# Performance work log

Measured on AMD Instinct MI355X. Metric: run time of the kernel, lower is better.

Reference implementation:

```python
import jax, jax.numpy as jnp
import numpy as np

N_TOKENS = 4096
EMBED = 2048
D_ATTN = 2048


def setup_inputs() -> dict:
    key = jax.random.key(0)
    k1, k2, k3, k4 = jax.random.split(key, 4)
    # torch.rand -> uniform [0,1); keeps scores positive so the multiplicative
    # -inf mask acts as a clean causal mask (faithful to original behavior).
    token_embeddings = jax.random.uniform(k1, (N_TOKENS, EMBED), dtype=jnp.float32)
    W_Q = jax.random.uniform(k2, (EMBED, D_ATTN), dtype=jnp.float32)
    W_K = jax.random.uniform(k3, (EMBED, D_ATTN), dtype=jnp.float32)
    W_V = jax.random.uniform(k4, (EMBED, D_ATTN), dtype=jnp.float32)
    return {"token_embeddings": token_embeddings, "W_Q": W_Q, "W_K": W_K, "W_V": W_V}


def reference(token_embeddings, W_Q, W_K, W_V):
    n = token_embeddings.shape[0]
    d = W_Q.shape[1]
    # mask: 1 on/below diagonal, -inf strictly above (multiplicative, as in source)
    neg_inf = jnp.float32(-jnp.inf)
    mask = jnp.tril(jnp.ones((n, n), dtype=jnp.float32)) + jnp.triu(
        jnp.full((n, n), neg_inf, dtype=jnp.float32), k=1
    )
    Q = token_embeddings @ W_Q          # (n, d)
    K = token_embeddings @ W_K          # (n, d)
    V = token_embeddings @ W_V          # (n, d)
    scores = (Q @ K.T) * mask           # (n, n); upper tri -> -inf (scores > 0)
    scores = scores / jnp.sqrt(jnp.float32(d))
    attn = jax.nn.softmax(scores, axis=-1)
    return attn @ V                     # (n, d)
```

## Files before the change

### kernel.cpp

```cpp
#include <hip/hip_runtime.h>
#include <hip/hip_bf16.h>
#include <cstdint>
#include <cstddef>
#include <cmath>

#define N_TOK 4096
#define EMB   2048
#define DATT  2048

typedef __attribute__((ext_vector_type(8))) short short8;
typedef __attribute__((ext_vector_type(4))) short shortx4;
typedef __attribute__((ext_vector_type(4))) float f32x4;

#define MFMA(a, b, c) __builtin_amdgcn_mfma_f32_16x16x32_bf16(a, b, c, 0, 0, 0)

__device__ __forceinline__ short f2bs(float f) {
  __hip_bfloat16 h = __float2bfloat16(f);
  return __builtin_bit_cast(short, h);
}
__device__ __forceinline__ float bs2f(short s) {
  return __uint_as_float(((unsigned)(unsigned short)s) << 16);
}
__device__ __forceinline__ float ldin(const void* p, size_t i, int isbf) {
  if (isbf) {
    unsigned short u = ((const unsigned short*)p)[i];
    return __uint_as_float(((unsigned int)u) << 16);
  }
  return ((const float*)p)[i];
}

__device__ __forceinline__ size_t swz(int r, int c, int kdim) {
  return ((size_t)((r >> 7) * (kdim >> 3) + (c >> 3)) << 10) +
         (size_t)((r & 127) << 3) + (c & 7);
}

__device__ __forceinline__ void gl16(const short* g, short* l) {
  __builtin_amdgcn_global_load_lds(
      (const __attribute__((address_space(1))) unsigned int*)(const void*)g,
      (__attribute__((address_space(3))) unsigned int*)(void*)l, 16, 0, 0);
}

template <bool THREE>
__device__ __forceinline__ void gemm_core(const short* Ah, const short* Al,
                                          const short* Bh, const short* Bl,
                                          int chunks, int apan, int bpan,
                                          int kmax, short* lds,
                                          f32x4 acc[4][4]) {
  const int NSL = THREE ? 4 : 2;
  int tid = threadIdx.x;
  int lane = tid & 63;
  int wave = tid >> 6;
  int ln = lane & 15, quad = lane >> 4;
  int wm = (wave >> 1) * 64, wn = (wave & 1) * 64;
  int wofs = wave * 512;

  auto stage = [&](int b, int k0) {
    size_t ao = ((size_t)(apan * chunks + (k0 >> 3))) << 10;
    size_t bo = ((size_t)(bpan * chunks + (k0 >> 3))) << 10;
    short* base = lds + b * NSL * 4096;
    const short* sa = Ah + ao + tid * 8;
    const short* sb = Bh + bo + tid * 8;
    gl16(sa,        base + wofs);
    gl16(sa + 2048, base + wofs + 2048);
    gl16(sb,        base + 4096 + wofs);
    gl16(sb + 2048, base + 4096 + wofs + 2048);
    if (THREE) {
      const short* sal = Al + ao + tid * 8;
      const short* sbl = Bl + bo + tid * 8;
      gl16(sal,        base + 8192 + wofs);
      gl16(sal + 2048, base + 8192 + wofs + 2048);
      gl16(sbl,        base + 12288 + wofs);
      gl16(sbl + 2048, base + 12288 + wofs + 2048);
    }
  };

  stage(0, 0);
  int cur = 0;
  int abase = quad * 1024 + (wm + ln) * 8;
  int bbase = quad * 1024 + (wn + ln) * 8;
  for (int k0 = 0; k0 < kmax; k0 += 32) {
    __syncthreads();
    if (k0 + 32 < kmax) stage(cur ^ 1, k0 + 32);
    const short* B0 = lds + cur * NSL * 4096;
    short8 fah[4], fbh[4];
#pragma unroll
    for (int i = 0; i < 4; ++i) fah[i] = *(const short8*)(B0 + abase + i * 128);
#pragma unroll
    for (int j = 0; j < 4; ++j) fbh[j] = *(const short8*)(B0 + 4096 + bbase + j * 128);
    if (THREE) {
      short8 fal[4], fbl[4];
#pragma unroll
      for (int i = 0; i < 4; ++i) fal[i] = *(const short8*)(B0 + 8192 + abase + i * 128);
#pragma unroll
      for (int j = 0; j < 4; ++j) fbl[j] = *(const short8*)(B0 + 12288 + bbase + j * 128);
#pragma unroll
      for (int j = 0; j < 4; ++j)
#pragma unroll
        for (int i = 0; i < 4; ++i) {
          acc[i][j] = MFMA(fah[i], fbh[j], acc[i][j]);
          acc[i][j] = MFMA(fah[i], fbl[j], acc[i][j]);
          acc[i][j] = MFMA(fal[i], fbh[j], acc[i][j]);
        }
    } else {
#pragma unroll
      for (int j = 0; j < 4; ++j)
#pragma unroll
        for (int i = 0; i < 4; ++i) acc[i][j] = MFMA(fah[i], fbh[j], acc[i][j]);
    }
    cur ^= 1;
  }
}

template <int AP, int BP>
__device__ __forceinline__ void gemm8(const short* __restrict__ Ah,
                                      const short* __restrict__ Al,
                                      const short* __restrict__ Bh,
                                      const short* __restrict__ Bl,
                                      int chunks, int apan, int bpan,
                                      int kmax, short* lds, f32x4 acc[4][4]) {
  constexpr int ASZ = AP * 4096;
  constexpr int BSZ = BP * 4096;
  constexpr int OAL = ASZ;
  constexpr int OBH = 2 * ASZ;
  constexpr int OBL = 2 * ASZ + BSZ;
  constexpr int BUF = 2 * ASZ + 2 * BSZ;
  constexpr int NNW = BP * 2;
  int tid = threadIdx.x;
  int lane = tid & 63, wave = tid >> 6;
  int ln = lane & 15, quad = lane >> 4;
  int wm = (wave / NNW) * 64, wn = (wave % NNW) * 64;
  int nt = kmax >> 5;

  auto sp = [&](int b, int t, int p) {
    short* base = lds + b * BUF;
    const short* g;
    short* l;
    if (p < AP)               { g = Ah + (((size_t)(apan + p) * chunks + (t << 2)) << 10);          l = base + p * 4096; }
    else if (p < 2 * AP)      { int q = p - AP;      g = Al + (((size_t)(apan + q) * chunks + (t << 2)) << 10); l = base + OAL + q * 4096; }
    else if (p < 2 * AP + BP) { int q = p - 2 * AP;  g = Bh + (((size_t)(bpan + q) * chunks + (t << 2)) << 10); l = base + OBH + q * 4096; }
    else                      { int q = p - 2 * AP - BP; g = Bl + (((size_t)(bpan + q) * chunks + (t << 2)) << 10); l = base + OBL + q * 4096; }
    gl16(g + tid * 8, l + wave * 512);
  };

#pragma unroll
  for (int p = 0; p < 6; ++p) sp(0, 0, p);
  if (nt > 1) {
#pragma unroll
    for (int p = 0; p < 6; ++p) sp(1, 1, p);
  }

  int abase = (wm & 128) * 32 + quad * 1024 + ((wm & 64) + ln) * 8;
  int bbase = (wn & 128) * 32 + quad * 1024 + ((wn & 64) + ln) * 8;
  int bi = 0;
  for (int t = 0; t < nt; ++t) {
    if (t + 1 < nt) asm volatile("s_waitcnt vmcnt(6)" ::: "memory");
    else            asm volatile("s_waitcnt vmcnt(0)" ::: "memory");
    __builtin_amdgcn_s_barrier();
    __builtin_amdgcn_sched_barrier(0);

    const short* L = lds + bi * BUF;
    int pi = bi + 2; if (pi > 2) pi -= 3;
    bool pf = (t + 2 < nt);

    short8 bh[4], bl[4];
#pragma unroll
    for (int j = 0; j < 4; ++j) {
      bh[j] = *(const short8*)(L + OBH + bbase + j * 128);
      bl[j] = *(const short8*)(L + OBL + bbase + j * 128);
    }
#pragma unroll
    for (int i = 0; i < 4; ++i) {
      short8 ah = *(const short8*)(L + abase + i * 128);
      short8 al = *(const short8*)(L + OAL + abase + i * 128);
      if (pf) {
        if (i == 0)      { sp(pi, t + 2, 0); sp(pi, t + 2, 1); }
        else if (i == 1) { sp(pi, t + 2, 2); sp(pi, t + 2, 3); }
        else if (i == 2) { sp(pi, t + 2, 4); }
        else             { sp(pi, t + 2, 5); }
      }
      __builtin_amdgcn_s_setprio(1);
#pragma unroll
      for (int j = 0; j < 4; ++j) {
        acc[i][j] = MFMA(ah, bh[j], acc[i][j]);
        acc[i][j] = MFMA(ah, bl[j], acc[i][j]);
        acc[i][j] = MFMA(al, bh[j], acc[i][j]);
      }
      __builtin_amdgcn_s_setprio(0);
    }
    ++bi; if (bi > 2) bi = 0;
  }
}

__device__ __forceinline__ void gemm1d2(const short* __restrict__ Ah,
                                        const short* __restrict__ Bh,
                                        int chunks, int apan, int bpan,
                                        int kmax, short* lds, f32x4 acc[4][4]) {
  int tid = threadIdx.x;
  int lane = tid & 63, wave = tid >> 6;
  int ln = lane & 15, quad = lane >> 4;
  int wm = (wave >> 1) * 64, wn = (wave & 1) * 64;
  int wofs = wave * 512;
  int nt = kmax >> 5;

  auto stage = [&](int b, int t) {
    size_t ao = ((size_t)(apan * chunks + (t << 2))) << 10;
    size_t bo = ((size_t)(bpan * chunks + (t << 2))) << 10;
    short* base = lds + b * 8192;
    gl16(Ah + ao + tid * 8,        base + wofs);
    gl16(Ah + ao + 2048 + tid * 8, base + wofs + 2048);
    gl16(Bh + bo + tid * 8,        base + 4096 + wofs);
    gl16(Bh + bo + 2048 + tid * 8, base + 4096 + wofs + 2048);
  };
  stage(0, 0);
  if (nt > 1) stage(1, 1);

  int abase = quad * 1024 + (wm + ln) * 8;
  int bbase = quad * 1024 + (wn + ln) * 8;
  int bi = 0;
  for (int t = 0; t < nt; ++t) {
    if (t + 1 < nt) asm volatile("s_waitcnt vmcnt(4)" ::: "memory");
    else            asm volatile("s_waitcnt vmcnt(0)" ::: "memory");
    __builtin_amdgcn_s_barrier();
    __builtin_amdgcn_sched_barrier(0);
    int pi = bi + 2; if (pi > 2) pi -= 3;
    if (t + 2 < nt) stage(pi, t + 2);
    const short* L = lds + bi * 8192;
    short8 fah[4], fbh[4];
#pragma unroll
    for (int i = 0; i < 4; ++i) fah[i] = *(const short8*)(L + abase + i * 128);
#pragma unroll
    for (int j = 0; j < 4; ++j) fbh[j] = *(const short8*)(L + 4096 + bbase + j * 128);
#pragma unroll
    for (int j = 0; j < 4; ++j)
#pragma unroll
      for (int i = 0; i < 4; ++i) acc[i][j] = MFMA(fah[i], fbh[j], acc[i][j]);
    ++bi; if (bi > 2) bi = 0;
  }
}

__global__ void k_sniff(const void* x, int* flag) {
  if (threadIdx.x == 0 && blockIdx.x == 0) {
    const unsigned short* u = (const unsigned short*)x;
    int bf = 1;
    for (int i = 0; i < 256; ++i) {
      unsigned short v = u[i];
      if ((v & 0x8000u) || ((v & 0x7FFFu) >= 0x3F80u)) { bf = 0; break; }
    }
    *flag = bf;
  }
}

__global__ __launch_bounds__(256) void k_xbar(const void* X, float* xbar,
                                              const int* flagp) {
  int isbf = *flagp;
  int e = blockIdx.x * 256 + threadIdx.x;
  float s = 0.f;
  for (int r = 0; r < 256; ++r) s += ldin(X, (size_t)r * EMB + e, isbf);
  xbar[e] = s * (1.f / 256.f);
}

__global__ __launch_bounds__(256) void k_split_x(const void* X, short* Xh, short* Xl,
                                                 const int* flagp) {
  int isbf = *flagp;
  size_t base = ((size_t)blockIdx.x * 256 + threadIdx.x) * 4;
  int r = (int)(base >> 11), c = (int)(base & 2047);
  shortx4 h, l;
#pragma unroll
  for (int u = 0; u < 4; ++u) {
    float x = ldin(X, base + u, isbf);
    short hh = f2bs(x);
    h[u] = hh;
    l[u] = f2bs(x - bs2f(hh));
  }
  size_t o = swz(r, c, EMB);
  *(shortx4*)(Xh + o) = h;
  *(shortx4*)(Xl + o) = l;
}

__global__ __launch_bounds__(256) void k_transpose_split(const void* W, short* Wth,
                                                         short* Wtl, int R, int C,
                                                         const int* flagp, int wlo) {
  __shared__ float T[64][65];
  int isbf = *flagp;
  int r0 = blockIdx.y * 64, c0 = blockIdx.x * 64;
  int tid = threadIdx.x;
#pragma unroll
  for (int it = 0; it < 16; ++it) {
    int idx = tid + it * 256;
    int row = idx >> 6, col = idx & 63;
    T[row][col] = ldin(W, (size_t)(r0 + row) * C + c0 + col, isbf);
  }
  __syncthreads();
#pragma unroll
  for (int it = 0; it < 16; ++it) {
    int idx = tid + it * 256;
    int row = idx >> 6, col = idx & 63;
    float x = T[col][row];
    short h = f2bs(x);
    size_t o = swz(c0 + row, r0 + col, R);
    Wth[o] = h;
    if (wlo) Wtl[o] = f2bs(x - bs2f(h));
  }
}

__global__ __launch_bounds__(256) void k_kbar(const short* Wth, const short* Wtl,
                                              const float* xbar, float* kbar) {
  int d = blockIdx.x;
  float s = 0.f;
  for (int e = threadIdx.x; e < EMB; e += 256) {
    size_t o = swz(d, e, EMB);
    s += xbar[e] * (bs2f(Wth[o]) + bs2f(Wtl[o]));
  }
  __shared__ float red[4];
#pragma unroll
  for (int off = 32; off > 0; off >>= 1) s += __shfl_down(s, off);
  if ((threadIdx.x & 63) == 0) red[threadIdx.x >> 6] = s;
  __syncthreads();
  if (threadIdx.x == 0) kbar[d] = red[0] + red[1] + red[2] + red[3];
}

__global__ __launch_bounds__(512, 2) void k_proj3(const short* Ah, const short* Al,
                                                  const short* Bh, const short* Bl,
                                                  short* Ch, short* Cl,
                                                  const float* bias) {
  __shared__ short lds[3 * 24576];
  int bid = blockIdx.x;
  int s = ((bid & 7) << 5) | (bid >> 3);
  int row0 = (s >> 4) << 8, col0 = (s & 15) << 7;
  f32x4 acc[4][4] = {};
  gemm8<2, 1>(Ah, Al, Bh, Bl, EMB >> 3, row0 >> 7, col0 >> 7, EMB, lds, acc);
  int tid = threadIdx.x;
  int wave = tid >> 6, lane = tid & 63;
  int ln = lane & 15, quad = lane >> 4;
  int wm = (wave >> 1) * 64, wn = (wave & 1) * 64;
#pragma unroll
  for (int i = 0; i < 4; ++i)
#pragma unroll
    for (int j = 0; j < 4; ++j)
#pragma unroll
      for (int r = 0; r < 4; ++r) {
        int row = row0 + wm + i * 16 + quad * 4 + r;
        int col = col0 + wn + j * 16 + ln;
        float x = acc[i][j][r];
        if (bias) x -= bias[col];
        short h = f2bs(x);
        size_t o = swz(row, col, DATT);
        Ch[o] = h;
        Cl[o] = f2bs(x - bs2f(h));
      }
}

__global__ __launch_bounds__(256, 3) void k_proj1(const short* Ah, const short* Bh,
                                                  short* Ch) {
  __shared__ short lds[3 * 8192];
  int bid = blockIdx.x;
  int s = ((bid & 7) << 6) | (bid >> 3);
  int row0 = (s >> 5) << 7, col0 = (s & 31) << 7;
  f32x4 acc[4][4] = {};
  gemm1d2(Ah, Bh, EMB >> 3, row0 >> 7, col0 >> 7, EMB, lds, acc);
  int tid = threadIdx.x;
  int wave = tid >> 6, lane = tid & 63;
  int ln = lane & 15, quad = lane >> 4;
  int wm = (wave >> 1) * 64, wn = (wave & 1) * 64;
#pragma unroll
  for (int i = 0; i < 4; ++i)
#pragma unroll
    for (int j = 0; j < 4; ++j)
#pragma unroll
      for (int r = 0; r < 4; ++r) {
        int row = row0 + wm + i * 16 + quad * 4 + r;
        int col = col0 + wn + j * 16 + ln;
        Ch[swz(row, col, N_TOK)] = f2bs(acc[i][j][r]);
      }
}

__global__ __launch_bounds__(256, 2) void k_score3(const short* Qh, const short* Ql,
                                                   const short* Kh, const short* Kl,
                                                   float* S) {
  int bi0 = blockIdx.x;
  int bi = (bi0 & 7) * 66 + (bi0 >> 3);
  int by = (int)((sqrtf(8.f * (float)bi + 1.f) - 1.f) * 0.5f);
  while ((by + 1) * (by + 2) / 2 <= bi) ++by;
  while (by * (by + 1) / 2 > bi) --by;
  int bx = bi - by * (by + 1) / 2;
  __shared__ short lds[2 * 16384];
  f32x4 acc[4][4] = {};
  gemm_core<true>(Qh, Ql, Kh, Kl, DATT >> 3, by, bx, DATT, lds, acc);
  int row0 = by * 128, col0 = bx * 128;
  int tid = threadIdx.x;
  int wave = tid >> 6, lane = tid & 63;
  int ln = lane & 15, quad = lane >> 4;
  int wm = (wave >> 1) * 64, wn = (wave & 1) * 64;
  const float scale = 0.022097086912079608f;
#pragma unroll
  for (int i = 0; i < 4; ++i)
#pragma unroll
    for (int j = 0; j < 4; ++j)
#pragma unroll
      for (int r = 0; r < 4; ++r) {
        int row = row0 + wm + i * 16 + quad * 4 + r;
        int col = col0 + wn + j * 16 + ln;
        if (col <= row) S[(size_t)row * N_TOK + col] = acc[i][j][r] * scale;
      }
}

__global__ __launch_bounds__(256) void k_softmax(const float* S, short* P) {
  int i = blockIdx.x;
  const float* row = S + (size_t)i * N_TOK;
  int len = i + 1;
  int tid = threadIdx.x;
  __shared__ float red[4];
  float m = -3.402823466e38f;
  for (int j = tid; j < len; j += 256) m = fmaxf(m, row[j]);
#pragma unroll
  for (int off = 32; off > 0; off >>= 1) m = fmaxf(m, __shfl_down(m, off));
  if ((tid & 63) == 0) red[tid >> 6] = m;
  __syncthreads();
  m = fmaxf(fmaxf(red[0], red[1]), fmaxf(red[2], red[3]));
  __syncthreads();
  float s = 0.f;
  for (int j = tid; j < len; j += 256) s += __expf(row[j] - m);
#pragma unroll
  for (int off = 32; off > 0; off >>= 1) s += __shfl_down(s, off);
  if ((tid & 63) == 0) red[tid >> 6] = s;
  __syncthreads();
  s = red[0] + red[1] + red[2] + red[3];
  float inv = 1.f / s;
  size_t rbase = ((size_t)(i >> 7) * (N_TOK >> 3) << 10) + (size_t)((i & 127) << 3);
  for (int j = tid; j < len; j += 256)
    P[rbase + ((size_t)(j >> 3) << 10) + (j & 7)] = f2bs(__expf(row[j] - m) * inv);
  int fillend = (len + 127) & ~127;
  for (int j = len + tid; j < fillend; j += 256)
    P[rbase + ((size_t)(j >> 3) << 10) + (j & 7)] = 0;
}

__global__ __launch_bounds__(256, 3) void k_out(const short* Ph, const short* Vh,
                                                void* Co, const int* flagp) {
  __shared__ short lds[3 * 8192];
  int bid = blockIdx.x;
  int half = bid >> 8;
  int r = bid & 255;
  int s = ((r & 7) << 5) | (r >> 3);
  int bb = s >> 4;
  int band = half ? bb : (31 - bb);
  int row0 = band << 7, col0 = (s & 15) << 7;
  f32x4 acc[4][4] = {};
  gemm1d2(Ph, Vh, N_TOK >> 3, row0 >> 7, col0 >> 7, row0 + 128, lds, acc);
  int isbf = *flagp;
  int tid = threadIdx.x;
  int wave = tid >> 6, lane = tid & 63;
  int ln = lane & 15, quad = lane >> 4;
  int wm = (wave >> 1) * 64, wn = (wave & 1) * 64;
#pragma unroll
  for (int i = 0; i < 4; ++i)
#pragma unroll
    for (int j = 0; j < 4; ++j)
#pragma unroll
      for (int r2 = 0; r2 < 4; ++r2) {
        int row = row0 + wm + i * 16 + quad * 4 + r2;
        int col = col0 + wn + j * 16 + ln;
        size_t idx = (size_t)row * DATT + col;
        if (isbf) ((__hip_bfloat16*)Co)[idx] = __float2bfloat16(acc[i][j][r2]);
        else      ((float*)Co)[idx] = acc[i][j][r2];
      }
}

extern "C" void kernel_launch(void* const* d_in, const int* in_sizes, int n_in,
                              void* d_out, int out_size, void* d_ws, size_t ws_size,
                              hipStream_t stream) {
  const void* X  = d_in[0];
  const void* WQ = d_in[1];
  const void* WK = d_in[2];
  const void* WV = d_in[3];

  float* ws   = (float*)d_ws;
  int*   flag = (int*)d_ws;
  float* xbar = ws + 256;
  float* kbar = ws + 2560;
  short* p0   = (short*)(ws + 16384);
  const size_t M8 = (size_t)N_TOK * DATT;
  const size_t M4 = (size_t)EMB * DATT;
  short* Xh  = p0;
  short* Xl  = Xh + M8;
  short* Wth = Xl + M8;
  short* Wtl = Wth + M4;
  float* S   = (float*)p0;
  short* Qh  = p0 + 4 * M8;
  short* Ql  = Qh + M8;
  short* Kh  = Ql + M8;
  short* Kl  = Kh + M8;
  short* Vt  = Kl + M8;
  short* P   = Qh;

  dim3 blk(256);
  dim3 blk512(512);

  k_sniff<<<1, 64, 0, stream>>>(X, flag);
  k_xbar<<<EMB / 256, blk, 0, stream>>>(X, xbar, flag);
  k_split_x<<<(N_TOK * EMB) / 1024, blk, 0, stream>>>(X, Xh, Xl, flag);

  dim3 gt(DATT / 64, EMB / 64);

  k_transpose_split<<<gt, blk, 0, stream>>>(WQ, Wth, Wtl, EMB, DATT, flag, 1);
  k_proj3<<<dim3(256), blk512, 0, stream>>>(Xh, Xl, Wth, Wtl, Qh, Ql, nullptr);
  k_transpose_split<<<gt, blk, 0, stream>>>(WK, Wth, Wtl, EMB, DATT, flag, 1);
  k_kbar<<<DATT, blk, 0, stream>>>(Wth, Wtl, xbar, kbar);
  k_proj3<<<dim3(256), blk512, 0, stream>>>(Xh, Xl, Wth, Wtl, Kh, Kl, kbar);
  k_transpose_split<<<gt, blk, 0, stream>>>(WV, Wth, nullptr, EMB, DATT, flag, 0);
  k_proj1<<<dim3(512), blk, 0, stream>>>(Wth, Xh, Vt);

  k_score3<<<dim3(528), blk, 0, stream>>>(Qh, Ql, Kh, Kl, S);

  k_softmax<<<N_TOK, blk, 0, stream>>>(S, P);

  k_out<<<dim3(512), blk, 0, stream>>>(P, Vt, d_out, flag);
}
```

Baseline: 630.6 us.

## Split softmax into online row-stat pass and tiled coalesced P write

Replaces the three-pass per-row softmax with a single-pass online max/sum kernel that stores each row's max and inverse sum. A second kernel, launched over lower-triangular 128x128 tiles, stages S through LDS and writes P into the blocked layout with vectorized 16-byte stores instead of scattered 2-byte stores. This cuts the reads of S from three passes to two and makes the P writes coalesced, at the cost of an extra launch, per-element rescaling exps in the online pass, and reading S a second time in the tile kernel.

```diff
diff --git a/kernel.cpp b/kernel.cpp
--- a/kernel.cpp
+++ b/kernel.cpp
@@ -404,34 +404,77 @@
       }
 }
 
-__global__ __launch_bounds__(256) void k_softmax(const float* S, short* P) {
+__global__ __launch_bounds__(256) void k_rowstat(const float* S, float2* RS) {
   int i = blockIdx.x;
   const float* row = S + (size_t)i * N_TOK;
   int len = i + 1;
   int tid = threadIdx.x;
-  __shared__ float red[4];
-  float m = -3.402823466e38f;
-  for (int j = tid; j < len; j += 256) m = fmaxf(m, row[j]);
-#pragma unroll
-  for (int off = 32; off > 0; off >>= 1) m = fmaxf(m, __shfl_down(m, off));
-  if ((tid & 63) == 0) red[tid >> 6] = m;
+  float m = -3.402823466e38f, s = 0.f;
+  for (int j = tid; j < len; j += 256) {
+    float x = row[j];
+    if (x > m) { s = s * __expf(m - x) + 1.f; m = x; }
+    else       { s += __expf(x - m); }
+  }
+#pragma unroll
+  for (int off = 32; off > 0; off >>= 1) {
+    float m2 = __shfl_down(m, off), s2 = __shfl_down(s, off);
+    float M = fmaxf(m, m2);
+    s = s * __expf(m - M) + s2 * __expf(m2 - M);
+    m = M;
+  }
+  __shared__ float rm[4], rs[4];
+  if ((tid & 63) == 0) { rm[tid >> 6] = m; rs[tid >> 6] = s; }
   __syncthreads();
-  m = fmaxf(fmaxf(red[0], red[1]), fmaxf(red[2], red[3]));
+  if (tid == 0) {
+#pragma unroll
+    for (int w = 1; w < 4; ++w) {
+      float M = fmaxf(m, rm[w]);
+      s = s * __expf(m - M) + rs[w] * __expf(rm[w] - M);
+      m = M;
+    }
+    RS[i] = make_float2(m, 1.f / s);
+  }
+}
+
+__global__ __launch_bounds__(256) void k_pwrite(const float* S, const float2* RS,
+                                                short* P) {
+  int bi = blockIdx.x;
+  int b = (int)((sqrtf(8.f * (float)bi + 1.f) - 1.f) * 0.5f);
+  while ((b + 1) * (b + 2) / 2 <= bi) ++b;
+  while (b * (b + 1) / 2 > bi) --b;
+  int c = bi - b * (b + 1) / 2;
+  int r0 = b << 7, c0 = c << 7;
+  __shared__ float T[128 * 130];
+  int tid = threadIdx.x;
+  {
+    int lane32 = tid & 31, rr0 = tid >> 5;
+#pragma unroll
+    for (int it = 0; it < 16; ++it) {
+      int rr = rr0 + it * 8;
+      const float4 v = *(const float4*)(S + (size_t)(r0 + rr) * N_TOK + c0 + lane32 * 4);
+      float* dst = T + rr * 130 + lane32 * 4;
+      dst[0] = v.x; dst[1] = v.y; dst[2] = v.z; dst[3] = v.w;
+    }
+  }
   __syncthreads();
-  float s = 0.f;
-  for (int j = tid; j < len; j += 256) s += __expf(row[j] - m);
-#pragma unroll
-  for (int off = 32; off > 0; off >>= 1) s += __shfl_down(s, off);
-  if ((tid & 63) == 0) red[tid >> 6] = s;
-  __syncthreads();
-  s = red[0] + red[1] + red[2] + red[3];
-  float inv = 1.f / s;
-  size_t rbase = ((size_t)(i >> 7) * (N_TOK >> 3) << 10) + (size_t)((i & 127) << 3);
-  for (int j = tid; j < len; j += 256)
-    P[rbase + ((size_t)(j >> 3) << 10) + (j & 7)] = f2bs(__expf(row[j] - m) * inv);
-  int fillend = (len + 127) & ~127;
-  for (int j = len + tid; j < fillend; j += 256)
-    P[rbase + ((size_t)(j >> 3) << 10) + (j & 7)] = 0;
+  int j = tid >> 4;
+  int rg = (tid & 15) << 3;
+  size_t chunk = (((size_t)(r0 >> 7) * (N_TOK >> 3) + (c0 >> 3) + j) << 10);
+  bool diag = (c == b);
+#pragma unroll
+  for (int k = 0; k < 8; ++k) {
+    int row = r0 + rg + k;
+    float2 ms = RS[row];
+    short8 out;
+#pragma unroll
+    for (int cc = 0; cc < 8; ++cc) {
+      float x = T[(rg + k) * 130 + j * 8 + cc];
+      float p = __expf(x - ms.x) * ms.y;
+      int col = c0 + j * 8 + cc;
+      out[cc] = (!diag || col <= row) ? f2bs(p) : (short)0;
+    }
+    *(short8*)(P + chunk + (size_t)(rg + k) * 8) = out;
+  }
 }
 
 __global__ __launch_bounds__(256, 3) void k_out(const short* Ph, const short* Vh,
@@ -477,6 +520,7 @@
   int*   flag = (int*)d_ws;
   float* xbar = ws + 256;
   float* kbar = ws + 2560;
+  float2* RS  = (float2*)(ws + 8192);
   short* p0   = (short*)(ws + 16384);
   const size_t M8 = (size_t)N_TOK * DATT;
   const size_t M4 = (size_t)EMB * DATT;
@@ -511,7 +555,8 @@
 
   k_score3<<<dim3(528), blk, 0, stream>>>(Qh, Ql, Kh, Kl, S);
 
-  k_softmax<<<N_TOK, blk, 0, stream>>>(S, P);
+  k_rowstat<<<dim3(N_TOK), blk, 0, stream>>>(S, RS);
+  k_pwrite<<<dim3(528), blk, 0, stream>>>(S, RS, P);
 
   k_out<<<dim3(512), blk, 0, stream>>>(P, Vt, d_out, flag);
 }
```

After: 635.3 us. No clear change (+0.7%).

## Load K fragments directly into registers in score kernel, stage only Q in LDS

Applied to the files above, without the earlier changes.

The triangular score GEMM now stages only the Q hi/lo panels in LDS through async global-to-LDS loads. The K hi/lo fragments are loaded straight from global memory into registers, double-buffered across two register sets. A manual vmcnt wait plus raw s_barrier and sched_barrier fences replace __syncthreads, and the MFMA block runs at raised wave priority. This halves LDS footprint and LDS read traffic and allows deeper overlap, at the cost of more VGPRs and fragile hand-tuned wait counts.

```diff
diff --git a/kernel.cpp b/kernel.cpp
--- a/kernel.cpp
+++ b/kernel.cpp
@@ -38,77 +38,6 @@
   __builtin_amdgcn_global_load_lds(
       (const __attribute__((address_space(1))) unsigned int*)(const void*)g,
       (__attribute__((address_space(3))) unsigned int*)(void*)l, 16, 0, 0);
-}
-
-template <bool THREE>
-__device__ __forceinline__ void gemm_core(const short* Ah, const short* Al,
-                                          const short* Bh, const short* Bl,
-                                          int chunks, int apan, int bpan,
-                                          int kmax, short* lds,
-                                          f32x4 acc[4][4]) {
-  const int NSL = THREE ? 4 : 2;
-  int tid = threadIdx.x;
-  int lane = tid & 63;
-  int wave = tid >> 6;
-  int ln = lane & 15, quad = lane >> 4;
-  int wm = (wave >> 1) * 64, wn = (wave & 1) * 64;
-  int wofs = wave * 512;
-
-  auto stage = [&](int b, int k0) {
-    size_t ao = ((size_t)(apan * chunks + (k0 >> 3))) << 10;
-    size_t bo = ((size_t)(bpan * chunks + (k0 >> 3))) << 10;
-    short* base = lds + b * NSL * 4096;
-    const short* sa = Ah + ao + tid * 8;
-    const short* sb = Bh + bo + tid * 8;
-    gl16(sa,        base + wofs);
-    gl16(sa + 2048, base + wofs + 2048);
-    gl16(sb,        base + 4096 + wofs);
-    gl16(sb + 2048, base + 4096 + wofs + 2048);
-    if (THREE) {
-      const short* sal = Al + ao + tid * 8;
-      const short* sbl = Bl + bo + tid * 8;
-      gl16(sal,        base + 8192 + wofs);
-      gl16(sal + 2048, base + 8192 + wofs + 2048);
-      gl16(sbl,        base + 12288 + wofs);
-      gl16(sbl + 2048, base + 12288 + wofs + 2048);
-    }
-  };
-
-  stage(0, 0);
-  int cur = 0;
-  int abase = quad * 1024 + (wm + ln) * 8;
-  int bbase = quad * 1024 + (wn + ln) * 8;
-  for (int k0 = 0; k0 < kmax; k0 += 32) {
-    __syncthreads();
-    if (k0 + 32 < kmax) stage(cur ^ 1, k0 + 32);
-    const short* B0 = lds + cur * NSL * 4096;
-    short8 fah[4], fbh[4];
-#pragma unroll
-    for (int i = 0; i < 4; ++i) fah[i] = *(const short8*)(B0 + abase + i * 128);
-#pragma unroll
-    for (int j = 0; j < 4; ++j) fbh[j] = *(const short8*)(B0 + 4096 + bbase + j * 128);
-    if (THREE) {
-      short8 fal[4], fbl[4];
-#pragma unroll
-      for (int i = 0; i < 4; ++i) fal[i] = *(const short8*)(B0 + 8192 + abase + i * 128);
-#pragma unroll
-      for (int j = 0; j < 4; ++j) fbl[j] = *(const short8*)(B0 + 12288 + bbase + j * 128);
-#pragma unroll
-      for (int j = 0; j < 4; ++j)
-#pragma unroll
-        for (int i = 0; i < 4; ++i) {
-          acc[i][j] = MFMA(fah[i], fbh[j], acc[i][j]);
-          acc[i][j] = MFMA(fah[i], fbl[j], acc[i][j]);
-          acc[i][j] = MFMA(fal[i], fbh[j], acc[i][j]);
-        }
-    } else {
-#pragma unroll
-      for (int j = 0; j < 4; ++j)
-#pragma unroll
-        for (int i = 0; i < 4; ++i) acc[i][j] = MFMA(fah[i], fbh[j], acc[i][j]);
-    }
-    cur ^= 1;
-  }
 }
 
 template <int AP, int BP>
@@ -383,14 +312,81 @@
   while ((by + 1) * (by + 2) / 2 <= bi) ++by;
   while (by * (by + 1) / 2 > bi) --by;
   int bx = bi - by * (by + 1) / 2;
-  __shared__ short lds[2 * 16384];
-  f32x4 acc[4][4] = {};
-  gemm_core<true>(Qh, Ql, Kh, Kl, DATT >> 3, by, bx, DATT, lds, acc);
-  int row0 = by * 128, col0 = bx * 128;
-  int tid = threadIdx.x;
-  int wave = tid >> 6, lane = tid & 63;
+  __shared__ short lds[2 * 8192];
+  int tid = threadIdx.x;
+  int lane = tid & 63, wave = tid >> 6;
   int ln = lane & 15, quad = lane >> 4;
   int wm = (wave >> 1) * 64, wn = (wave & 1) * 64;
+  int wofs = wave * 512;
+  const int chunks = DATT >> 3;
+  const short8* B8h = (const short8*)Kh + (size_t)bx * (chunks * 128);
+  const short8* B8l = (const short8*)Kl + (size_t)bx * (chunks * 128);
+  int abase = quad * 1024 + (wm + ln) * 8;
+  f32x4 acc[4][4] = {};
+
+  auto stageA = [&](int b, int t) {
+    size_t ao = ((size_t)(by * chunks + (t << 2)) << 10);
+    short* base = lds + b * 8192;
+    gl16(Qh + ao + tid * 8,        base + wofs);
+    gl16(Qh + ao + 2048 + tid * 8, base + wofs + 2048);
+    gl16(Ql + ao + tid * 8,        base + 4096 + wofs);
+    gl16(Ql + ao + 2048 + tid * 8, base + 4096 + wofs + 2048);
+  };
+
+  short8 bh0[4], bl0[4], bh1[4], bl1[4];
+  auto loadB = [&](int t, short8 (&BH)[4], short8 (&BL)[4]) {
+    int tq = (t << 2) + quad;
+#pragma unroll
+    for (int j = 0; j < 4; ++j) {
+      BH[j] = B8h[(size_t)tq * 128 + wn + j * 16 + ln];
+      BL[j] = B8l[(size_t)tq * 128 + wn + j * 16 + ln];
+    }
+  };
+
+  auto tile = [&](int cb, short8 (&BH)[4], short8 (&BL)[4], bool pf, int tn,
+                  short8 (&BHn)[4], short8 (&BLn)[4]) {
+    asm volatile("s_waitcnt vmcnt(8)" ::: "memory");
+    __builtin_amdgcn_s_barrier();
+    __builtin_amdgcn_sched_barrier(0);
+    if (pf) {
+      stageA(cb ^ 1, tn);
+      __builtin_amdgcn_sched_barrier(0);
+      loadB(tn, BHn, BLn);
+      __builtin_amdgcn_sched_barrier(0);
+    }
+    const short* L = lds + cb * 8192;
+    short8 fah[4], fal[4];
+#pragma unroll
+    for (int i = 0; i < 4; ++i) {
+      fah[i] = *(const short8*)(L + abase + i * 128);
+      fal[i] = *(const short8*)(L + 4096 + abase + i * 128);
+    }
+    __builtin_amdgcn_s_setprio(1);
+#pragma unroll
+    for (int j = 0; j < 4; ++j)
+#pragma unroll
+      for (int i = 0; i < 4; ++i) {
+        acc[i][j] = MFMA(fah[i], BH[j], acc[i][j]);
+        acc[i][j] = MFMA(fah[i], BL[j], acc[i][j]);
+        acc[i][j] = MFMA(fal[i], BH[j], acc[i][j]);
+      }
+    __builtin_amdgcn_s_setprio(0);
+  };
+
+  stageA(0, 0);
+  __builtin_amdgcn_sched_barrier(0);
+  loadB(0, bh0, bl0);
+  const int nt = DATT >> 5;
+  int cur = 0;
+  for (int t = 0; t < nt; t += 2) {
+    tile(cur, bh0, bl0, true, t + 1, bh1, bl1);
+    cur ^= 1;
+    bool pf = (t + 2 < nt);
+    tile(cur, bh1, bl1, pf, t + 2, bh0, bl0);
+    cur ^= 1;
+  }
+
+  int row0 = by * 128, col0 = bx * 128;
   const float scale = 0.022097086912079608f;
 #pragma unroll
   for (int i = 0; i < 4; ++i)
@@ -511,7 +507,7 @@
 
   k_score3<<<dim3(528), blk, 0, stream>>>(Qh, Ql, Kh, Kl, S);
 
-  k_softmax<<<N_TOK, blk, 0, stream>>>(S, P);
+  k_softmax<<<dim3(N_TOK), blk, 0, stream>>>(S, P);
 
   k_out<<<dim3(512), blk, 0, stream>>>(P, Vt, d_out, flag);
 }
```

Measured after the change: 644.5 us. +2.2%, slower.
